# Kernel optimization log

Hardware: AMD Instinct MI355X
Metric: run time of the kernel (lower is better)

Reference implementation:

```python
import jax, jax.numpy as jnp
import numpy as np


def conv1x1(x, w, b):
    # x: [B,C,H,W], w: [O,C], b: [O]
    return jnp.einsum('oc,bchw->bohw', w, x) + b[None, :, None, None]


def interp_bilinear_ac(x, oh, ow):
    # bilinear resize with align_corners=True, x: [B,C,H,W] -> [B,C,oh,ow]
    B, C, H, W = x.shape
    if (H, W) == (oh, ow):
        return x
    ys = jnp.linspace(0.0, H - 1.0, oh)
    xs = jnp.linspace(0.0, W - 1.0, ow)
    y0 = jnp.clip(jnp.floor(ys).astype(jnp.int32), 0, H - 1)
    y1 = jnp.minimum(y0 + 1, H - 1)
    x0 = jnp.clip(jnp.floor(xs).astype(jnp.int32), 0, W - 1)
    x1 = jnp.minimum(x0 + 1, W - 1)
    wy = (ys - y0).astype(x.dtype)
    wx = (xs - x0).astype(x.dtype)
    top = x[:, :, y0, :] * (1 - wy)[None, None, :, None] + x[:, :, y1, :] * wy[None, None, :, None]
    out = top[:, :, :, x0] * (1 - wx)[None, None, None, :] + top[:, :, :, x1] * wx[None, None, None, :]
    return out


def non_local(x, qw, qb, kw, kb, vw, vb, ow_, ob):
    B, C, H, W = x.shape
    HW = H * W
    q = conv1x1(x, qw, qb).reshape(B, -1, HW)  # [B, Ci, HW]
    k = conv1x1(x, kw, kb).reshape(B, -1, HW)
    v = conv1x1(x, vw, vb).reshape(B, -1, HW)
    attn = jnp.einsum('bci,bcj->bij', q, k)     # [B, HW, HW]
    attn = jax.nn.softmax(attn, axis=-1)
    out = jnp.einsum('bcj,bij->bci', v, attn)   # [B, Ci, HW]
    out = out.reshape(B, -1, H, W)
    return conv1x1(out, ow_, ob)


def _forward(x1, x2, x3, x4, qw, qb, kw, kb, vw, vb, ow_, ob, g1w, g1b, g2w, g2b):
    H1, W1 = x1.shape[2], x1.shape[3]
    x2_up = interp_bilinear_ac(x2, H1, W1)
    x3_up = interp_bilinear_ac(x3, H1, W1)
    x4_up = interp_bilinear_ac(x4, H1, W1)
    gf = jnp.concatenate([x1, x2_up, x3_up, x4_up], axis=1)  # [B, 128, H1, W1]
    gf = non_local(gf, qw, qb, kw, kb, vw, vb, ow_, ob)
    h = jax.nn.relu(conv1x1(gf, g1w, g1b))
    sw = jax.nn.sigmoid(conv1x1(h, g2w, g2b))                # [B, 128, H1, W1]
    w1, w2, w3, w4 = sw[:, :32], sw[:, 32:64], sw[:, 64:96], sw[:, 96:128]
    x1_out = x1 * (1 + w1)
    x2_out = x2 * (1 + interp_bilinear_ac(w2, x2.shape[2], x2.shape[3]))
    x3_out = x3 * (1 + interp_bilinear_ac(w3, x3.shape[2], x3.shape[3]))
    x4_out = x4 * (1 + interp_bilinear_ac(w4, x4.shape[2], x4.shape[3]))
    return (x1_out, x2_out, x3_out, x4_out)


def setup_inputs() -> dict:
    key = jax.random.key(0)
    ks = jax.random.split(key, 16)
    C = 128  # channel*4
    Ci = 64  # inter_channel
    Cg = 32
    d = {
        'x1': jax.random.normal(ks[0], (8, 32, 64, 64), jnp.float32),
        'x2': jax.random.normal(ks[1], (8, 32, 32, 32), jnp.float32),
        'x3': jax.random.normal(ks[2], (8, 32, 16, 16), jnp.float32),
        'x4': jax.random.normal(ks[3], (8, 32, 8, 8), jnp.float32),
        'qw': jax.random.normal(ks[4], (Ci, C), jnp.float32) * 0.05,
        'qb': jnp.zeros((Ci,), jnp.float32),
        'kw': jax.random.normal(ks[5], (Ci, C), jnp.float32) * 0.05,
        'kb': jnp.zeros((Ci,), jnp.float32),
        'vw': jax.random.normal(ks[6], (Ci, C), jnp.float32) * 0.05,
        'vb': jnp.zeros((Ci,), jnp.float32),
        'ow_': jax.random.normal(ks[7], (C, Ci), jnp.float32) * 0.05,
        'ob': jnp.zeros((C,), jnp.float32),
        'g1w': jax.random.normal(ks[8], (Cg, C), jnp.float32) * 0.05,
        'g1b': jnp.zeros((Cg,), jnp.float32),
        'g2w': jax.random.normal(ks[9], (C, Cg), jnp.float32) * 0.05,
        'g2b': jnp.zeros((C,), jnp.float32),
    }
    return d


def reference(x1, x2, x3, x4, qw, qb, kw, kb, vw, vb, ow_, ob, g1w, g1b, g2w, g2b):
    return _forward(x1, x2, x3, x4, qw, qb, kw, kb, vw, vb, ow_, ob, g1w, g1b, g2w, g2b)
```

## Files before the change

### kernel.cpp

```cpp
#include <hip/hip_runtime.h>
#include <hip/hip_bf16.h>


typedef __attribute__((ext_vector_type(8))) short s16x8;
typedef __attribute__((ext_vector_type(4))) float f32x4;

#define LOG2E 1.44269504088896340736f

__device__ __forceinline__ unsigned int f2bf(float f) {
    unsigned int u = __float_as_uint(f);
    u += 0x7fffu + ((u >> 16) & 1u);
    return u >> 16;
}
__device__ __forceinline__ unsigned int pk2bf(float a, float b) {
    union { __hip_bfloat162 h; unsigned int u; } cv;
    cv.h = __float22bfloat162_rn(make_float2(a, b));
    return cv.u;
}
__device__ __forceinline__ float bf2f(unsigned short u) {
    return __uint_as_float((unsigned int)u << 16);
}
__device__ __forceinline__ float fexp2(float x) {
    return __builtin_amdgcn_exp2f(x);
}
__device__ __forceinline__ float frcp(float x) {
    return __builtin_amdgcn_rcpf(x);
}

__global__ __launch_bounds__(256) void k_prep(
    const float* __restrict__ qw, const float* __restrict__ qb,
    const float* __restrict__ kw, const float* __restrict__ kb,
    const float* __restrict__ vw, const float* __restrict__ vb,
    const float* __restrict__ ow, const float* __restrict__ g1w,
    const float* __restrict__ g2w,
    unsigned short* __restrict__ WTb, float* __restrict__ bqkv,
    unsigned short* __restrict__ owb, unsigned short* __restrict__ g1wb,
    unsigned short* __restrict__ g2wb) {
  int t = blockIdx.x * 256 + threadIdx.x;
  if (t < 192 * 128) {
    int oc = t >> 7, c = t & 127;
    float v;
    if (oc < 64)       v = qw[oc * 128 + c] * LOG2E;
    else if (oc < 128) v = kw[(oc - 64) * 128 + c];
    else               v = vw[(oc - 128) * 128 + c];
    WTb[t] = (unsigned short)f2bf(v);
  }
  if (t < 192) {
    float v;
    if (t < 64)       v = qb[t] * LOG2E;
    else if (t < 128) v = kb[t - 64];
    else              v = vb[t - 128];
    bqkv[t] = v;
  }
  if (t < 128 * 64) g1wb[t & 4095] = (unsigned short)f2bf(g1w[t & 4095]);
  if (t < 128 * 64) owb[t] = (unsigned short)f2bf(ow[t]);
  if (t < 128 * 32) g2wb[t] = (unsigned short)f2bf(g2w[t]);
}

__global__ __launch_bounds__(256) void k_qkv(
    const float* __restrict__ x1, const float* __restrict__ x2,
    const float* __restrict__ x3, const float* __restrict__ x4,
    const unsigned short* __restrict__ WTb, const float* __restrict__ bqkv,
    unsigned short* __restrict__ Qg, unsigned short* __restrict__ Kg,
    unsigned short* __restrict__ Vg) {
  __shared__ __align__(16) unsigned short gfb[64 * 136];
  unsigned int* gfbu = (unsigned int*)gfb;

  const int b = blockIdx.x >> 6;
  const int i0 = (blockIdx.x & 63) << 6;
  const int t = threadIdx.x;

  {
    const int cp = t >> 2, q = t & 3;
    const int c0 = cp << 1;
    const int pbase = q << 4;
    const int oy = i0 >> 6;
    const int ox0 = pbase;

    if (cp < 16) {
      const float* s0 = x1 + (((b * 32 + c0) << 12) + (oy << 6) + ox0);
      const float* s1 = s0 + 4096;
      #pragma unroll
      for (int k4 = 0; k4 < 4; k4++) {
        float4 va = ((const float4*)s0)[k4];
        float4 vb = ((const float4*)s1)[k4];
        int p = pbase + k4 * 4;
        gfbu[(p + 0) * 68 + cp] = pk2bf(va.x, vb.x);
        gfbu[(p + 1) * 68 + cp] = pk2bf(va.y, vb.y);
        gfbu[(p + 2) * 68 + cp] = pk2bf(va.z, vb.z);
        gfbu[(p + 3) * 68 + cp] = pk2bf(va.w, vb.w);
      }
    } else {
      const float* base; int S, cs;
      if (cp < 32)      { base = x2; S = 32; cs = c0 - 32; }
      else if (cp < 48) { base = x3; S = 16; cs = c0 - 64; }
      else              { base = x4; S = 8;  cs = c0 - 96; }
      const float* pl0 = base + (b * 32 + cs) * S * S;
      const float* pl1 = pl0 + S * S;
      float yf = (float)oy * (float)(S - 1) * (1.0f / 63.0f);
      int y0 = (int)yf; if (y0 > S - 1) y0 = S - 1;
      int y1 = y0 + 1;  if (y1 > S - 1) y1 = S - 1;
      float wy = yf - (float)y0;
      const float* r00 = pl0 + y0 * S; const float* r01 = pl0 + y1 * S;
      const float* r10 = pl1 + y0 * S; const float* r11 = pl1 + y1 * S;
      for (int k = 0; k < 16; k++) {
        int ox = ox0 + k;
        float xf = (float)ox * (float)(S - 1) * (1.0f / 63.0f);
        int xx0 = (int)xf; if (xx0 > S - 1) xx0 = S - 1;
        int xx1 = xx0 + 1; if (xx1 > S - 1) xx1 = S - 1;
        float wx = xf - (float)xx0;
        float a0 = r00[xx0] + wx * (r00[xx1] - r00[xx0]);
        float b0 = r01[xx0] + wx * (r01[xx1] - r01[xx0]);
        float v0 = a0 + wy * (b0 - a0);
        float a1 = r10[xx0] + wx * (r10[xx1] - r10[xx0]);
        float b1 = r11[xx0] + wx * (r11[xx1] - r11[xx0]);
        float v1 = a1 + wy * (b1 - a1);
        gfbu[(pbase + k) * 68 + cp] = pk2bf(v0, v1);
      }
    }
  }
  __syncthreads();

  const int wv = t >> 6, lane = t & 63;
  const int r = lane & 15, qd = lane >> 4;
  const int ocb = wv * 48;

  s16x8 af[3][4];
  #pragma unroll
  for (int mti = 0; mti < 3; mti++)
    #pragma unroll
    for (int ks = 0; ks < 4; ks++)
      af[mti][ks] = *(const s16x8*)&WTb[(ocb + mti * 16 + r) * 128 + ks * 32 + qd * 8];
  float4 bias[3];
  #pragma unroll
  for (int mti = 0; mti < 3; mti++)
    bias[mti] = *(const float4*)&bqkv[ocb + mti * 16 + qd * 4];

  f32x4 zf = {0.f, 0.f, 0.f, 0.f};
  #pragma unroll 1
  for (int nt = 0; nt < 4; nt++) {
    s16x8 bfr[4];
    #pragma unroll
    for (int ks = 0; ks < 4; ks++)
      bfr[ks] = *(const s16x8*)&gfb[(nt * 16 + r) * 136 + ks * 32 + qd * 8];
    f32x4 acc[3] = {zf, zf, zf};
    #pragma unroll
    for (int ks = 0; ks < 4; ks++)
      #pragma unroll
      for (int mti = 0; mti < 3; mti++)
        acc[mti] = __builtin_amdgcn_mfma_f32_16x16x32_bf16(af[mti][ks], bfr[ks], acc[mti], 0, 0, 0);

    const int pos = i0 + nt * 16 + r;
    #pragma unroll
    for (int mti = 0; mti < 3; mti++) {
      const int gmt = wv * 3 + mti;
      float ax = acc[mti].x + bias[mti].x;
      float ay = acc[mti].y + bias[mti].y;
      float az = acc[mti].z + bias[mti].z;
      float aw = acc[mti].w + bias[mti].w;
      if (gmt < 4) {
        uint2 w; w.x = pk2bf(ax, ay); w.y = pk2bf(az, aw);
        *(uint2*)&Qg[(((b << 12) + pos) << 6) + gmt * 16 + qd * 4] = w;
      } else if (gmt < 8) {
        uint2 w; w.x = pk2bf(ax, ay); w.y = pk2bf(az, aw);
        *(uint2*)&Kg[(((b << 12) + pos) << 6) + (gmt - 4) * 16 + qd * 4] = w;
      } else {
        int ocv = (gmt - 8) * 16 + qd * 4;
        Vg[((b * 64 + ocv + 0) << 12) + pos] = (unsigned short)f2bf(ax);
        Vg[((b * 64 + ocv + 1) << 12) + pos] = (unsigned short)f2bf(ay);
        Vg[((b * 64 + ocv + 2) << 12) + pos] = (unsigned short)f2bf(az);
        Vg[((b * 64 + ocv + 3) << 12) + pos] = (unsigned short)f2bf(aw);
      }
    }
  }
}

__global__ __launch_bounds__(256, 4) void k_attn(
    const unsigned short* __restrict__ Qg, const unsigned short* __restrict__ Kg,
    const unsigned short* __restrict__ Vg, unsigned short* __restrict__ Op,
    float* __restrict__ Lp) {
  __shared__ __align__(16) unsigned short Kl[64 * 72];
  __shared__ __align__(16) unsigned short Vl[64 * 72];
  __shared__ __align__(16) unsigned short Pl[4][32 * 72];

  const int b = blockIdx.x >> 7;
  const int part = (blockIdx.x >> 5) & 3;
  const int qg = blockIdx.x & 31;
  const int i0 = qg << 7;
  const int t = threadIdx.x;
  const int wv = t >> 6, lane = t & 63;
  const int r = lane & 15, qd = lane >> 4;
  const int qbase = i0 + wv * 32;

  s16x8 qf[2][2];
  #pragma unroll
  for (int nt = 0; nt < 2; nt++)
    #pragma unroll
    for (int ks = 0; ks < 2; ks++)
      qf[nt][ks] = *(const s16x8*)&Qg[(((b << 12) + qbase + nt * 16 + r) << 6) + ks * 32 + qd * 8];

  f32x4 zf = {0.f, 0.f, 0.f, 0.f};
  f32x4 acc[2][4];
  #pragma unroll
  for (int nt = 0; nt < 2; nt++)
    #pragma unroll
    for (int mt = 0; mt < 4; mt++) acc[nt][mt] = zf;
  f32x4 accl[2] = {zf, zf};

  const short ob = (r == 0) ? (short)0x3F80 : (short)0;
  const s16x8 vones = {ob, ob, ob, ob, ob, ob, ob, ob};

  const int srow = t >> 3, sseg = t & 7;
  const unsigned short* kt0 = &Kg[(((b << 12) + (part << 10) + srow) << 6) + sseg * 8];
  const unsigned short* vt0 = &Vg[((b * 64 + srow) << 12) + (part << 10) + sseg * 8];
  uint4 pk0 = *(const uint4*)(kt0);
  uint4 pk1 = *(const uint4*)(kt0 + (32 << 6));
  uint4 pv0 = *(const uint4*)(vt0);
  uint4 pv1 = *(const uint4*)(vt0 + (32 << 12));

  for (int it = 0; it < 16; it++) {
    __syncthreads();
    *(uint4*)&Kl[srow * 72 + sseg * 8] = pk0;
    *(uint4*)&Kl[(srow + 32) * 72 + sseg * 8] = pk1;
    *(uint4*)&Vl[srow * 72 + sseg * 8] = pv0;
    *(uint4*)&Vl[(srow + 32) * 72 + sseg * 8] = pv1;
    __syncthreads();
    if (it < 15) {
      int j0 = (it + 1) << 6;
      pk0 = *(const uint4*)(kt0 + (j0 << 6));
      pk1 = *(const uint4*)(kt0 + ((j0 + 32) << 6));
      pv0 = *(const uint4*)(vt0 + j0);
      pv1 = *(const uint4*)(vt0 + (32 << 12) + j0);
    }

    #pragma unroll
    for (int mt = 0; mt < 4; mt++) {
      s16x8 kf0 = *(const s16x8*)&Kl[(mt * 16 + r) * 72 + qd * 8];
      s16x8 kf1 = *(const s16x8*)&Kl[(mt * 16 + r) * 72 + 32 + qd * 8];
      #pragma unroll
      for (int nt = 0; nt < 2; nt++) {
        f32x4 s = __builtin_amdgcn_mfma_f32_16x16x32_bf16(kf0, qf[nt][0], zf, 0, 0, 0);
        s = __builtin_amdgcn_mfma_f32_16x16x32_bf16(kf1, qf[nt][1], s, 0, 0, 0);
        float px = fexp2(fminf(s.x, 80.f));
        float py = fexp2(fminf(s.y, 80.f));
        float pz = fexp2(fminf(s.z, 80.f));
        float pw = fexp2(fminf(s.w, 80.f));
        uint2 w;
        w.x = pk2bf(px, py);
        w.y = pk2bf(pz, pw);
        *(uint2*)&Pl[wv][(nt * 16 + r) * 72 + mt * 16 + qd * 4] = w;
      }
    }
    __builtin_amdgcn_wave_barrier();

    #pragma unroll
    for (int ks = 0; ks < 2; ks++) {
      s16x8 pf0 = *(const s16x8*)&Pl[wv][(r) * 72 + ks * 32 + qd * 8];
      s16x8 pf1 = *(const s16x8*)&Pl[wv][(16 + r) * 72 + ks * 32 + qd * 8];
      #pragma unroll
      for (int mt = 0; mt < 4; mt++) {
        s16x8 vf = *(const s16x8*)&Vl[(mt * 16 + r) * 72 + ks * 32 + qd * 8];
        acc[0][mt] = __builtin_amdgcn_mfma_f32_16x16x32_bf16(vf, pf0, acc[0][mt], 0, 0, 0);
        acc[1][mt] = __builtin_amdgcn_mfma_f32_16x16x32_bf16(vf, pf1, acc[1][mt], 0, 0, 0);
      }
      accl[0] = __builtin_amdgcn_mfma_f32_16x16x32_bf16(vones, pf0, accl[0], 0, 0, 0);
      accl[1] = __builtin_amdgcn_mfma_f32_16x16x32_bf16(vones, pf1, accl[1], 0, 0, 0);
    }
  }

  #pragma unroll
  for (int nt = 0; nt < 2; nt++) {
    float lv = __shfl(accl[nt].x, r);
    float inv = frcp(lv);
    int qrow = qbase + nt * 16 + r;
    unsigned short* orow = &Op[(((part * 8 + b) << 12) + qrow) << 6];
    #pragma unroll
    for (int mt = 0; mt < 4; mt++) {
      uint2 w;
      w.x = pk2bf(acc[nt][mt].x * inv, acc[nt][mt].y * inv);
      w.y = pk2bf(acc[nt][mt].z * inv, acc[nt][mt].w * inv);
      *(uint2*)&orow[mt * 16 + qd * 4] = w;
    }
    if (qd == 0) Lp[((part * 8 + b) << 12) + qrow] = lv;
  }
}

__global__ __launch_bounds__(256) void k_out(
    const unsigned short* __restrict__ Op, const float* __restrict__ Lp,
    const unsigned short* __restrict__ owb, const float* __restrict__ obias,
    const unsigned short* __restrict__ g1wb, const float* __restrict__ g1b,
    const unsigned short* __restrict__ g2wb, const float* __restrict__ g2b,
    unsigned short* __restrict__ SWb) {
  __shared__ __align__(16) unsigned short Ot[128 * 72];
  __shared__ __align__(16) unsigned short gf2t[128 * 136];
  __shared__ __align__(16) unsigned short ht[128 * 40];
  const int b = blockIdx.x >> 5;
  const int i0 = (blockIdx.x & 31) << 7;
  const int t = threadIdx.x;

  {
    const int pos = t >> 1, half = t & 1;
    const int i = i0 + pos;
    float lp4[4], lsum = 0.f;
    #pragma unroll
    for (int p = 0; p < 4; p++) { lp4[p] = Lp[((p * 8 + b) << 12) + i]; lsum += lp4[p]; }
    float o[32];
    #pragma unroll
    for (int k = 0; k < 32; k++) o[k] = 0.f;
    float invs = frcp(lsum);
    #pragma unroll
    for (int p = 0; p < 4; p++) {
      float w = lp4[p] * invs;
      const uint2* prow = (const uint2*)&Op[((((p * 8 + b) << 12) + i) << 6) + half * 32];
      #pragma unroll
      for (int k = 0; k < 8; k++) {
        uint2 u = prow[k];
        o[k * 4 + 0] += w * __uint_as_float(u.x << 16);
        o[k * 4 + 1] += w * __uint_as_float(u.x & 0xFFFF0000u);
        o[k * 4 + 2] += w * __uint_as_float(u.y << 16);
        o[k * 4 + 3] += w * __uint_as_float(u.y & 0xFFFF0000u);
      }
    }
    unsigned int* dst = (unsigned int*)&Ot[pos * 72 + half * 32];
    #pragma unroll
    for (int k = 0; k < 16; k++) dst[k] = pk2bf(o[2 * k], o[2 * k + 1]);
  }
  __syncthreads();

  const int wv = t >> 6, lane = t & 63;
  const int r = lane & 15, qd = lane >> 4;
  f32x4 zf = {0.f, 0.f, 0.f, 0.f};

  {
    const int ocb = wv * 32;
    s16x8 af[2][2];
    #pragma unroll
    for (int mt = 0; mt < 2; mt++)
      #pragma unroll
      for (int ks = 0; ks < 2; ks++)
        af[mt][ks] = *(const s16x8*)&owb[(ocb + mt * 16 + r) * 64 + ks * 32 + qd * 8];
    float4 bias[2];
    #pragma unroll
    for (int mt = 0; mt < 2; mt++)
      bias[mt] = *(const float4*)&obias[ocb + mt * 16 + qd * 4];
    #pragma unroll 1
    for (int nt = 0; nt < 8; nt++) {
      s16x8 bfr[2];
      #pragma unroll
      for (int ks = 0; ks < 2; ks++)
        bfr[ks] = *(const s16x8*)&Ot[(nt * 16 + r) * 72 + ks * 32 + qd * 8];
      f32x4 acc[2] = {zf, zf};
      #pragma unroll
      for (int ks = 0; ks < 2; ks++)
        #pragma unroll
        for (int mt = 0; mt < 2; mt++)
          acc[mt] = __builtin_amdgcn_mfma_f32_16x16x32_bf16(af[mt][ks], bfr[ks], acc[mt], 0, 0, 0);
      #pragma unroll
      for (int mt = 0; mt < 2; mt++) {
        uint2 w;
        w.x = pk2bf(acc[mt].x + bias[mt].x, acc[mt].y + bias[mt].y);
        w.y = pk2bf(acc[mt].z + bias[mt].z, acc[mt].w + bias[mt].w);
        *(uint2*)&gf2t[(nt * 16 + r) * 136 + ocb + mt * 16 + qd * 4] = w;
      }
    }
  }
  __syncthreads();

  {
    s16x8 af[2][4];
    #pragma unroll
    for (int mt = 0; mt < 2; mt++)
      #pragma unroll
      for (int ks = 0; ks < 4; ks++)
        af[mt][ks] = *(const s16x8*)&g1wb[(mt * 16 + r) * 128 + ks * 32 + qd * 8];
    float4 bias[2];
    #pragma unroll
    for (int mt = 0; mt < 2; mt++)
      bias[mt] = *(const float4*)&g1b[mt * 16 + qd * 4];
    #pragma unroll
    for (int nt = 0; nt < 2; nt++) {
      const int pn = (wv * 2 + nt) * 16 + r;
      s16x8 bfr[4];
      #pragma unroll
      for (int ks = 0; ks < 4; ks++)
        bfr[ks] = *(const s16x8*)&gf2t[pn * 136 + ks * 32 + qd * 8];
      f32x4 acc[2] = {zf, zf};
      #pragma unroll
      for (int ks = 0; ks < 4; ks++)
        #pragma unroll
        for (int mt = 0; mt < 2; mt++)
          acc[mt] = __builtin_amdgcn_mfma_f32_16x16x32_bf16(af[mt][ks], bfr[ks], acc[mt], 0, 0, 0);
      #pragma unroll
      for (int mt = 0; mt < 2; mt++) {
        uint2 w;
        w.x = pk2bf(fmaxf(acc[mt].x + bias[mt].x, 0.f), fmaxf(acc[mt].y + bias[mt].y, 0.f));
        w.y = pk2bf(fmaxf(acc[mt].z + bias[mt].z, 0.f), fmaxf(acc[mt].w + bias[mt].w, 0.f));
        *(uint2*)&ht[pn * 40 + mt * 16 + qd * 4] = w;
      }
    }
  }
  __syncthreads();

  {
    const int nb = wv * 32;
    s16x8 bfg[2];
    float bias[2];
    #pragma unroll
    for (int ntl = 0; ntl < 2; ntl++) {
      bfg[ntl] = *(const s16x8*)&g2wb[(nb + ntl * 16 + r) * 32 + qd * 8];
      bias[ntl] = g2b[nb + ntl * 16 + r];
    }
    #pragma unroll 1
    for (int mt = 0; mt < 8; mt++) {
      s16x8 af = *(const s16x8*)&ht[(mt * 16 + r) * 40 + qd * 8];
      #pragma unroll
      for (int ntl = 0; ntl < 2; ntl++) {
        f32x4 acc = __builtin_amdgcn_mfma_f32_16x16x32_bf16(af, bfg[ntl], zf, 0, 0, 0);
        const int oc3 = nb + ntl * 16 + r;
        float s0 = frcp(1.0f + fexp2(-LOG2E * (acc.x + bias[ntl])));
        float s1 = frcp(1.0f + fexp2(-LOG2E * (acc.y + bias[ntl])));
        float s2 = frcp(1.0f + fexp2(-LOG2E * (acc.z + bias[ntl])));
        float s3 = frcp(1.0f + fexp2(-LOG2E * (acc.w + bias[ntl])));
        uint2 w; w.x = pk2bf(s0, s1); w.y = pk2bf(s2, s3);
        *(uint2*)&SWb[((b * 128 + oc3) << 12) + i0 + mt * 16 + qd * 4] = w;
      }
    }
  }
}

__device__ __forceinline__ float bilin64(const unsigned short* __restrict__ p,
                                         int oy, int ox, int n) {
  float yf = (float)oy * 63.0f / (float)n;
  int y0 = (int)yf; if (y0 > 63) y0 = 63;
  int y1 = y0 + 1;  if (y1 > 63) y1 = 63;
  float wy = yf - (float)y0;
  float xf = (float)ox * 63.0f / (float)n;
  int x0 = (int)xf; if (x0 > 63) x0 = 63;
  int x1 = x0 + 1;  if (x1 > 63) x1 = 63;
  float wx = xf - (float)x0;
  float v00 = bf2f(p[y0 * 64 + x0]), v01 = bf2f(p[y0 * 64 + x1]);
  float v10 = bf2f(p[y1 * 64 + x0]), v11 = bf2f(p[y1 * 64 + x1]);
  float top = v00 + wx * (v01 - v00);
  float bot = v10 + wx * (v11 - v10);
  return top + wy * (bot - top);
}

__global__ __launch_bounds__(256) void k_final(
    const float* __restrict__ x1, const float* __restrict__ x2,
    const float* __restrict__ x3, const float* __restrict__ x4,
    const unsigned short* __restrict__ SWb, float* __restrict__ out) {
  const int N1 = 1048576, N2 = 262144, N3 = 65536, N4 = 16384;
  int idx = blockIdx.x * 256 + threadIdx.x;
  if (idx < N1) {
    int b = idx >> 17, rr = idx & 131071;
    int c = rr >> 12, hw = rr & 4095;
    out[idx] = x1[idx] * (1.f + bf2f(SWb[((b * 128 + c) << 12) + hw]));
  } else if (idx < N1 + N2) {
    int i2 = idx - N1;
    int b = i2 >> 15, rr = i2 & 32767;
    int c = rr >> 10, oy = (rr >> 5) & 31, ox = rr & 31;
    float w = bilin64(SWb + ((b * 128 + 32 + c) << 12), oy, ox, 31);
    out[idx] = x2[i2] * (1.f + w);
  } else if (idx < N1 + N2 + N3) {
    int i3 = idx - N1 - N2;
    int b = i3 >> 13, rr = i3 & 8191;
    int c = rr >> 8, oy = (rr >> 4) & 15, ox = rr & 15;
    float w = bilin64(SWb + ((b * 128 + 64 + c) << 12), oy, ox, 15);
    out[idx] = x3[i3] * (1.f + w);
  } else if (idx < N1 + N2 + N3 + N4) {
    int i4 = idx - N1 - N2 - N3;
    int b = i4 >> 11, rr = i4 & 2047;
    int c = rr >> 6, oy = (rr >> 3) & 7, ox = rr & 7;
    float w = bilin64(SWb + ((b * 128 + 96 + c) << 12), oy, ox, 7);
    out[idx] = x4[i4] * (1.f + w);
  }
}

extern "C" void kernel_launch(void* const* d_in, const int* in_sizes, int n_in,
                              void* d_out, int out_size, void* d_ws, size_t ws_size,
                              hipStream_t stream) {
  const float* x1  = (const float*)d_in[0];
  const float* x2  = (const float*)d_in[1];
  const float* x3  = (const float*)d_in[2];
  const float* x4  = (const float*)d_in[3];
  const float* qw  = (const float*)d_in[4];
  const float* qb  = (const float*)d_in[5];
  const float* kw  = (const float*)d_in[6];
  const float* kb  = (const float*)d_in[7];
  const float* vw  = (const float*)d_in[8];
  const float* vb  = (const float*)d_in[9];
  const float* ow  = (const float*)d_in[10];
  const float* ob  = (const float*)d_in[11];
  const float* g1w = (const float*)d_in[12];
  const float* g1b = (const float*)d_in[13];
  const float* g2w = (const float*)d_in[14];
  const float* g2b = (const float*)d_in[15];
  float* out = (float*)d_out;

  char* ws = (char*)d_ws;
  unsigned short* Qg  = (unsigned short*)(ws + 0);
  unsigned short* Kg  = (unsigned short*)(ws + 4194304);
  unsigned short* Vg  = (unsigned short*)(ws + 8388608);
  unsigned short* SWb = (unsigned short*)(ws + 0);
  unsigned short* Op  = (unsigned short*)(ws + 12582912);
  float* Lp   = (float*)(ws + 29360128);
  unsigned short* WTb = (unsigned short*)(ws + 29884416);
  float* bqkv = (float*)(ws + 29933568);
  unsigned short* owb  = (unsigned short*)(ws + 29934592);
  unsigned short* g1wb = (unsigned short*)(ws + 29950976);
  unsigned short* g2wb = (unsigned short*)(ws + 29959168);

  k_prep<<<96, 256, 0, stream>>>(qw, qb, kw, kb, vw, vb, ow, g1w, g2w,
                                 WTb, bqkv, owb, g1wb, g2wb);
  k_qkv<<<512, 256, 0, stream>>>(x1, x2, x3, x4, WTb, bqkv, Qg, Kg, Vg);
  k_attn<<<1024, 256, 0, stream>>>(Qg, Kg, Vg, Op, Lp);
  k_out<<<256, 256, 0, stream>>>(Op, Lp, owb, ob, g1wb, g1b, g2wb, g2b, SWb);
  k_final<<<5440, 256, 0, stream>>>(x1, x2, x3, x4, SWb, out);
}
```

Measured before the change: 184.4 us.

## Fuse weight conversion into consumers, halve k_out tile, fuse x1 gating

Removes the k_prep launch: each consumer kernel now loads fp32 weights directly and converts them to bf16 in registers, with the log2e scale folded into the Q weights and bias. k_out now handles 64 positions per block instead of 128 and doubles its grid. It also applies the x1 gating directly, so the first 32 sigmoid channels never go through SWb, and k_final only covers x2 through x4. This drops one launch and the SWb round trip for x1. The cost is redundant per-block weight conversion and more blocks each reloading the weights.

```diff
diff --git a/kernel.cpp b/kernel.cpp
--- a/kernel.cpp
+++ b/kernel.cpp
@@ -26,41 +26,23 @@
 __device__ __forceinline__ float frcp(float x) {
     return __builtin_amdgcn_rcpf(x);
 }
-
-__global__ __launch_bounds__(256) void k_prep(
+__device__ __forceinline__ s16x8 cvt8(const float* __restrict__ p, float scale) {
+    float4 a = ((const float4*)p)[0];
+    float4 b = ((const float4*)p)[1];
+    union { s16x8 v; uint4 u; } cv;
+    cv.u.x = pk2bf(a.x * scale, a.y * scale);
+    cv.u.y = pk2bf(a.z * scale, a.w * scale);
+    cv.u.z = pk2bf(b.x * scale, b.y * scale);
+    cv.u.w = pk2bf(b.z * scale, b.w * scale);
+    return cv.v;
+}
+
+__global__ __launch_bounds__(256) void k_qkv(
+    const float* __restrict__ x1, const float* __restrict__ x2,
+    const float* __restrict__ x3, const float* __restrict__ x4,
     const float* __restrict__ qw, const float* __restrict__ qb,
     const float* __restrict__ kw, const float* __restrict__ kb,
     const float* __restrict__ vw, const float* __restrict__ vb,
-    const float* __restrict__ ow, const float* __restrict__ g1w,
-    const float* __restrict__ g2w,
-    unsigned short* __restrict__ WTb, float* __restrict__ bqkv,
-    unsigned short* __restrict__ owb, unsigned short* __restrict__ g1wb,
-    unsigned short* __restrict__ g2wb) {
-  int t = blockIdx.x * 256 + threadIdx.x;
-  if (t < 192 * 128) {
-    int oc = t >> 7, c = t & 127;
-    float v;
-    if (oc < 64)       v = qw[oc * 128 + c] * LOG2E;
-    else if (oc < 128) v = kw[(oc - 64) * 128 + c];
-    else               v = vw[(oc - 128) * 128 + c];
-    WTb[t] = (unsigned short)f2bf(v);
-  }
-  if (t < 192) {
-    float v;
-    if (t < 64)       v = qb[t] * LOG2E;
-    else if (t < 128) v = kb[t - 64];
-    else              v = vb[t - 128];
-    bqkv[t] = v;
-  }
-  if (t < 128 * 64) g1wb[t & 4095] = (unsigned short)f2bf(g1w[t & 4095]);
-  if (t < 128 * 64) owb[t] = (unsigned short)f2bf(ow[t]);
-  if (t < 128 * 32) g2wb[t] = (unsigned short)f2bf(g2w[t]);
-}
-
-__global__ __launch_bounds__(256) void k_qkv(
-    const float* __restrict__ x1, const float* __restrict__ x2,
-    const float* __restrict__ x3, const float* __restrict__ x4,
-    const unsigned short* __restrict__ WTb, const float* __restrict__ bqkv,
     unsigned short* __restrict__ Qg, unsigned short* __restrict__ Kg,
     unsigned short* __restrict__ Vg) {
   __shared__ __align__(16) unsigned short gfb[64 * 136];
@@ -126,15 +108,20 @@
   const int ocb = wv * 48;
 
   s16x8 af[3][4];
-  #pragma unroll
-  for (int mti = 0; mti < 3; mti++)
-    #pragma unroll
-    for (int ks = 0; ks < 4; ks++)
-      af[mti][ks] = *(const s16x8*)&WTb[(ocb + mti * 16 + r) * 128 + ks * 32 + qd * 8];
   float4 bias[3];
   #pragma unroll
-  for (int mti = 0; mti < 3; mti++)
-    bias[mti] = *(const float4*)&bqkv[ocb + mti * 16 + qd * 4];
+  for (int mti = 0; mti < 3; mti++) {
+    const int goc = ocb + mti * 16;
+    const float* wsrc; const float* bsrc; float scale;
+    if (goc < 64)       { wsrc = qw + goc * 128;         bsrc = qb + goc;         scale = LOG2E; }
+    else if (goc < 128) { wsrc = kw + (goc - 64) * 128;  bsrc = kb + (goc - 64);  scale = 1.0f; }
+    else                { wsrc = vw + (goc - 128) * 128; bsrc = vb + (goc - 128); scale = 1.0f; }
+    #pragma unroll
+    for (int ks = 0; ks < 4; ks++)
+      af[mti][ks] = cvt8(wsrc + r * 128 + ks * 32 + qd * 8, scale);
+    float4 bv = *(const float4*)(bsrc + qd * 4);
+    bias[mti] = make_float4(bv.x * scale, bv.y * scale, bv.z * scale, bv.w * scale);
+  }
 
   f32x4 zf = {0.f, 0.f, 0.f, 0.f};
   #pragma unroll 1
@@ -287,33 +274,34 @@
 
 __global__ __launch_bounds__(256) void k_out(
     const unsigned short* __restrict__ Op, const float* __restrict__ Lp,
-    const unsigned short* __restrict__ owb, const float* __restrict__ obias,
-    const unsigned short* __restrict__ g1wb, const float* __restrict__ g1b,
-    const unsigned short* __restrict__ g2wb, const float* __restrict__ g2b,
+    const float* __restrict__ ow, const float* __restrict__ obias,
+    const float* __restrict__ g1w, const float* __restrict__ g1b,
+    const float* __restrict__ g2w, const float* __restrict__ g2b,
+    const float* __restrict__ x1, float* __restrict__ out,
     unsigned short* __restrict__ SWb) {
-  __shared__ __align__(16) unsigned short Ot[128 * 72];
-  __shared__ __align__(16) unsigned short gf2t[128 * 136];
-  __shared__ __align__(16) unsigned short ht[128 * 40];
-  const int b = blockIdx.x >> 5;
-  const int i0 = (blockIdx.x & 31) << 7;
+  __shared__ __align__(16) unsigned short Ot[64 * 72];
+  __shared__ __align__(16) unsigned short gf2t[64 * 136];
+  __shared__ __align__(16) unsigned short ht[64 * 40];
+  const int b = blockIdx.x >> 6;
+  const int i0 = (blockIdx.x & 63) << 6;
   const int t = threadIdx.x;
 
   {
-    const int pos = t >> 1, half = t & 1;
+    const int pos = t >> 2, q4 = t & 3;
     const int i = i0 + pos;
     float lp4[4], lsum = 0.f;
     #pragma unroll
     for (int p = 0; p < 4; p++) { lp4[p] = Lp[((p * 8 + b) << 12) + i]; lsum += lp4[p]; }
-    float o[32];
-    #pragma unroll
-    for (int k = 0; k < 32; k++) o[k] = 0.f;
+    float o[16];
+    #pragma unroll
+    for (int k = 0; k < 16; k++) o[k] = 0.f;
     float invs = frcp(lsum);
     #pragma unroll
     for (int p = 0; p < 4; p++) {
       float w = lp4[p] * invs;
-      const uint2* prow = (const uint2*)&Op[((((p * 8 + b) << 12) + i) << 6) + half * 32];
-      #pragma unroll
-      for (int k = 0; k < 8; k++) {
+      const uint2* prow = (const uint2*)&Op[((((p * 8 + b) << 12) + i) << 6) + q4 * 16];
+      #pragma unroll
+      for (int k = 0; k < 4; k++) {
         uint2 u = prow[k];
         o[k * 4 + 0] += w * __uint_as_float(u.x << 16);
         o[k * 4 + 1] += w * __uint_as_float(u.x & 0xFFFF0000u);
@@ -321,9 +309,9 @@
         o[k * 4 + 3] += w * __uint_as_float(u.y & 0xFFFF0000u);
       }
     }
-    unsigned int* dst = (unsigned int*)&Ot[pos * 72 + half * 32];
-    #pragma unroll
-    for (int k = 0; k < 16; k++) dst[k] = pk2bf(o[2 * k], o[2 * k + 1]);
+    unsigned int* dst = (unsigned int*)&Ot[pos * 72 + q4 * 16];
+    #pragma unroll
+    for (int k = 0; k < 8; k++) dst[k] = pk2bf(o[2 * k], o[2 * k + 1]);
   }
   __syncthreads();
 
@@ -338,13 +326,13 @@
     for (int mt = 0; mt < 2; mt++)
       #pragma unroll
       for (int ks = 0; ks < 2; ks++)
-        af[mt][ks] = *(const s16x8*)&owb[(ocb + mt * 16 + r) * 64 + ks * 32 + qd * 8];
+        af[mt][ks] = cvt8(&ow[(ocb + mt * 16 + r) * 64 + ks * 32 + qd * 8], 1.0f);
     float4 bias[2];
     #pragma unroll
     for (int mt = 0; mt < 2; mt++)
       bias[mt] = *(const float4*)&obias[ocb + mt * 16 + qd * 4];
     #pragma unroll 1
-    for (int nt = 0; nt < 8; nt++) {
+    for (int nt = 0; nt < 4; nt++) {
       s16x8 bfr[2];
       #pragma unroll
       for (int ks = 0; ks < 2; ks++)
@@ -372,31 +360,28 @@
     for (int mt = 0; mt < 2; mt++)
       #pragma unroll
       for (int ks = 0; ks < 4; ks++)
-        af[mt][ks] = *(const s16x8*)&g1wb[(mt * 16 + r) * 128 + ks * 32 + qd * 8];
+        af[mt][ks] = cvt8(&g1w[(mt * 16 + r) * 128 + ks * 32 + qd * 8], 1.0f);
     float4 bias[2];
     #pragma unroll
     for (int mt = 0; mt < 2; mt++)
       bias[mt] = *(const float4*)&g1b[mt * 16 + qd * 4];
-    #pragma unroll
-    for (int nt = 0; nt < 2; nt++) {
-      const int pn = (wv * 2 + nt) * 16 + r;
-      s16x8 bfr[4];
-      #pragma unroll
-      for (int ks = 0; ks < 4; ks++)
-        bfr[ks] = *(const s16x8*)&gf2t[pn * 136 + ks * 32 + qd * 8];
-      f32x4 acc[2] = {zf, zf};
-      #pragma unroll
-      for (int ks = 0; ks < 4; ks++)
-        #pragma unroll
-        for (int mt = 0; mt < 2; mt++)
-          acc[mt] = __builtin_amdgcn_mfma_f32_16x16x32_bf16(af[mt][ks], bfr[ks], acc[mt], 0, 0, 0);
-      #pragma unroll
-      for (int mt = 0; mt < 2; mt++) {
-        uint2 w;
-        w.x = pk2bf(fmaxf(acc[mt].x + bias[mt].x, 0.f), fmaxf(acc[mt].y + bias[mt].y, 0.f));
-        w.y = pk2bf(fmaxf(acc[mt].z + bias[mt].z, 0.f), fmaxf(acc[mt].w + bias[mt].w, 0.f));
-        *(uint2*)&ht[pn * 40 + mt * 16 + qd * 4] = w;
-      }
+    const int pn = wv * 16 + r;
+    s16x8 bfr[4];
+    #pragma unroll
+    for (int ks = 0; ks < 4; ks++)
+      bfr[ks] = *(const s16x8*)&gf2t[pn * 136 + ks * 32 + qd * 8];
+    f32x4 acc[2] = {zf, zf};
+    #pragma unroll
+    for (int ks = 0; ks < 4; ks++)
+      #pragma unroll
+      for (int mt = 0; mt < 2; mt++)
+        acc[mt] = __builtin_amdgcn_mfma_f32_16x16x32_bf16(af[mt][ks], bfr[ks], acc[mt], 0, 0, 0);
+    #pragma unroll
+    for (int mt = 0; mt < 2; mt++) {
+      uint2 w;
+      w.x = pk2bf(fmaxf(acc[mt].x + bias[mt].x, 0.f), fmaxf(acc[mt].y + bias[mt].y, 0.f));
+      w.y = pk2bf(fmaxf(acc[mt].z + bias[mt].z, 0.f), fmaxf(acc[mt].w + bias[mt].w, 0.f));
+      *(uint2*)&ht[pn * 40 + mt * 16 + qd * 4] = w;
     }
   }
   __syncthreads();
@@ -407,11 +392,11 @@
     float bias[2];
     #pragma unroll
     for (int ntl = 0; ntl < 2; ntl++) {
-      bfg[ntl] = *(const s16x8*)&g2wb[(nb + ntl * 16 + r) * 32 + qd * 8];
+      bfg[ntl] = cvt8(&g2w[(nb + ntl * 16 + r) * 32 + qd * 8], 1.0f);
       bias[ntl] = g2b[nb + ntl * 16 + r];
     }
     #pragma unroll 1
-    for (int mt = 0; mt < 8; mt++) {
+    for (int mt = 0; mt < 4; mt++) {
       s16x8 af = *(const s16x8*)&ht[(mt * 16 + r) * 40 + qd * 8];
       #pragma unroll
       for (int ntl = 0; ntl < 2; ntl++) {
@@ -421,8 +406,17 @@
         float s1 = frcp(1.0f + fexp2(-LOG2E * (acc.y + bias[ntl])));
         float s2 = frcp(1.0f + fexp2(-LOG2E * (acc.z + bias[ntl])));
         float s3 = frcp(1.0f + fexp2(-LOG2E * (acc.w + bias[ntl])));
-        uint2 w; w.x = pk2bf(s0, s1); w.y = pk2bf(s2, s3);
-        *(uint2*)&SWb[((b * 128 + oc3) << 12) + i0 + mt * 16 + qd * 4] = w;
+        if (nb == 0) {
+          const int off = ((b * 32 + oc3) << 12) + i0 + mt * 16 + qd * 4;
+          float4 xv = *(const float4*)&x1[off];
+          float4 o4;
+          o4.x = xv.x * (1.f + s0); o4.y = xv.y * (1.f + s1);
+          o4.z = xv.z * (1.f + s2); o4.w = xv.w * (1.f + s3);
+          *(float4*)&out[off] = o4;
+        } else {
+          uint2 w; w.x = pk2bf(s0, s1); w.y = pk2bf(s2, s3);
+          *(uint2*)&SWb[((b * 128 + oc3) << 12) + i0 + mt * 16 + qd * 4] = w;
+        }
       }
     }
   }
@@ -446,33 +440,28 @@
 }
 
 __global__ __launch_bounds__(256) void k_final(
-    const float* __restrict__ x1, const float* __restrict__ x2,
-    const float* __restrict__ x3, const float* __restrict__ x4,
+    const float* __restrict__ x2, const float* __restrict__ x3,
+    const float* __restrict__ x4,
     const unsigned short* __restrict__ SWb, float* __restrict__ out) {
   const int N1 = 1048576, N2 = 262144, N3 = 65536, N4 = 16384;
   int idx = blockIdx.x * 256 + threadIdx.x;
-  if (idx < N1) {
-    int b = idx >> 17, rr = idx & 131071;
-    int c = rr >> 12, hw = rr & 4095;
-    out[idx] = x1[idx] * (1.f + bf2f(SWb[((b * 128 + c) << 12) + hw]));
-  } else if (idx < N1 + N2) {
-    int i2 = idx - N1;
-    int b = i2 >> 15, rr = i2 & 32767;
+  if (idx < N2) {
+    int b = idx >> 15, rr = idx & 32767;
     int c = rr >> 10, oy = (rr >> 5) & 31, ox = rr & 31;
     float w = bilin64(SWb + ((b * 128 + 32 + c) << 12), oy, ox, 31);
-    out[idx] = x2[i2] * (1.f + w);
-  } else if (idx < N1 + N2 + N3) {
-    int i3 = idx - N1 - N2;
+    out[N1 + idx] = x2[idx] * (1.f + w);
+  } else if (idx < N2 + N3) {
+    int i3 = idx - N2;
     int b = i3 >> 13, rr = i3 & 8191;
     int c = rr >> 8, oy = (rr >> 4) & 15, ox = rr & 15;
     float w = bilin64(SWb + ((b * 128 + 64 + c) << 12), oy, ox, 15);
-    out[idx] = x3[i3] * (1.f + w);
-  } else if (idx < N1 + N2 + N3 + N4) {
-    int i4 = idx - N1 - N2 - N3;
+    out[N1 + idx] = x3[i3] * (1.f + w);
+  } else if (idx < N2 + N3 + N4) {
+    int i4 = idx - N2 - N3;
     int b = i4 >> 11, rr = i4 & 2047;
     int c = rr >> 6, oy = (rr >> 3) & 7, ox = rr & 7;
     float w = bilin64(SWb + ((b * 128 + 96 + c) << 12), oy, ox, 7);
-    out[idx] = x4[i4] * (1.f + w);
+    out[N1 + idx] = x4[i4] * (1.f + w);
   }
 }
 
@@ -504,16 +493,11 @@
   unsigned short* SWb = (unsigned short*)(ws + 0);
   unsigned short* Op  = (unsigned short*)(ws + 12582912);
   float* Lp   = (float*)(ws + 29360128);
-  unsigned short* WTb = (unsigned short*)(ws + 29884416);
-  float* bqkv = (float*)(ws + 29933568);
-  unsigned short* owb  = (unsigned short*)(ws + 29934592);
-  unsigned short* g1wb = (unsigned short*)(ws + 29950976);
-  unsigned short* g2wb = (unsigned short*)(ws + 29959168);
-
-  k_prep<<<96, 256, 0, stream>>>(qw, qb, kw, kb, vw, vb, ow, g1w, g2w,
-                                 WTb, bqkv, owb, g1wb, g2wb);
-  k_qkv<<<512, 256, 0, stream>>>(x1, x2, x3, x4, WTb, bqkv, Qg, Kg, Vg);
+
+  k_qkv<<<512, 256, 0, stream>>>(x1, x2, x3, x4, qw, qb, kw, kb, vw, vb,
+                                 Qg, Kg, Vg);
   k_attn<<<1024, 256, 0, stream>>>(Qg, Kg, Vg, Op, Lp);
-  k_out<<<256, 256, 0, stream>>>(Op, Lp, owb, ob, g1wb, g1b, g2wb, g2b, SWb);
-  k_final<<<5440, 256, 0, stream>>>(x1, x2, x3, x4, SWb, out);
-}
+  k_out<<<512, 256, 0, stream>>>(Op, Lp, ow, ob, g1w, g1b, g2w, g2b,
+                                 x1, out, SWb);
+  k_final<<<1344, 256, 0, stream>>>(x2, x3, x4, SWb, out);
+}
```

Result: no change. 187.5 us (+1.7%).
